# Kernel optimization log

Measured on AMD Instinct MI355X. Metric: run time of the kernel, lower is better.

## Reference

```python
import jax, jax.numpy as jnp
import numpy as np

N_NODES = 100000
D_FEAT = 128            # per-embedding width; concat of 4 -> 512
INPUT_DIM = 4 * D_FEAT
HIDDEN_DIM = 64
N_SAMPLES = 250000


def _glorot(key, fan_in, fan_out):
    r = np.sqrt(6.0 / fan_in).astype(np.float32)
    return jax.random.uniform(key, (fan_in, fan_out), minval=-r, maxval=r, dtype=jnp.float32)


def setup_inputs() -> dict:
    key = jax.random.key(0)
    k1, k2, k3, k4, k5 = jax.random.split(key, 5)
    input1 = jax.random.normal(k1, (N_NODES, D_FEAT), dtype=jnp.float32)
    input2 = jax.random.normal(k2, (N_NODES, D_FEAT), dtype=jnp.float32)
    train_sample = jax.random.randint(k3, (N_SAMPLES, 2), 0, N_NODES, dtype=jnp.int64)
    w1 = _glorot(k4, INPUT_DIM, HIDDEN_DIM)
    b1 = jnp.zeros((HIDDEN_DIM,), dtype=jnp.float32)
    w2 = _glorot(k5, HIDDEN_DIM, 1)
    return {"input1": input1, "input2": input2, "train_sample": train_sample,
            "w1": w1, "b1": b1, "w2": w2}


def reference(input1, input2, train_sample, w1, b1, w2):
    src = train_sample[:, 0]
    dst = train_sample[:, 1]
    # four gathers + concat -> [E, 4*D_FEAT]
    h = jnp.concatenate([input1[src], input1[dst], input2[src], input2[dst]], axis=1)
    x = jax.nn.relu(h @ w1 + b1)          # [E, HIDDEN_DIM]
    return x @ w2                          # [E, 1]
```

## Files before the change

kernel.cpp:

```cpp
#include <hip/hip_runtime.h>
#include <hip/hip_bf16.h>

#define NN  100000
#define DF  128
#define HD  64
#define NS  250000


typedef __attribute__((ext_vector_type(8))) short bfrag;
typedef __attribute__((ext_vector_type(4))) float ffrag;

__device__ __forceinline__ unsigned short bf16bits(float f) {
    __hip_bfloat16 b = __float2bfloat16(f);
    return *(unsigned short*)&b;
}
__device__ __forceinline__ unsigned pack2(float a, float b) {
    return (unsigned)bf16bits(a) | ((unsigned)bf16bits(b) << 16);
}
__device__ __forceinline__ float bflo(unsigned u) {
    union { unsigned i; float f; } c; c.i = u << 16; return c.f;
}
__device__ __forceinline__ float bfhi(unsigned u) {
    union { unsigned i; float f; } c; c.i = u & 0xffff0000u; return c.f;
}

__global__ __launch_bounds__(256) void prep_w1_kernel(
    const float* __restrict__ w1, const float* __restrict__ w2,
    unsigned short* __restrict__ Bf, unsigned short* __restrict__ w2bf)
{
    const int gid = blockIdx.x * 256 + threadIdx.x;
    if (gid >= 4096) {
        const int j = gid - 4096;
        if (j < HD) w2bf[j] = bf16bits(w2[j]);
        return;
    }
    const int lane = gid & 63;
    const int ks   = (gid >> 6) & 7;
    const int tn   = gid >> 9;

    const int n     = tn * 16 + (lane & 15);
    const int kbase = ks * 32 + (lane >> 4) * 8;
    const int col   = n & 63;

    uint4 u;
    unsigned p[4];
    #pragma unroll
    for (int jp = 0; jp < 4; ++jp) {
        float v[2];
        #pragma unroll
        for (int h = 0; h < 2; ++h) {
            const int k = kbase + jp * 2 + h;
            const int row = ((k >= 128) ? 256 : 0) + ((n >= 64) ? 128 : 0) + (k & 127);
            v[h] = w1[(size_t)row * HD + col];
        }
        p[jp] = pack2(v[0], v[1]);
    }
    u.x = p[0]; u.y = p[1]; u.z = p[2]; u.w = p[3];
    *(uint4*)(Bf + (size_t)gid * 8) = u;
}

__global__ __launch_bounds__(256) void node_gemm_mfma(
    const float* __restrict__ in1,
    const float* __restrict__ in2,
    const unsigned short* __restrict__ Bf,
    const float* __restrict__ b1,
    unsigned short* __restrict__ Pn)
{
    __shared__ unsigned short smem[20480];

    const int t  = threadIdx.x;
    const int m0 = blockIdx.x * 80;

    const int lane = t & 63;
    const int w    = t >> 6;
    bfrag bfr[2][8];
    #pragma unroll
    for (int ti = 0; ti < 2; ++ti) {
        const int tn = w * 2 + ti;
        #pragma unroll
        for (int ks = 0; ks < 8; ++ks)
            bfr[ti][ks] = *(const bfrag*)(Bf + ((size_t)(tn * 8 + ks) * 64 + lane) * 8);
    }

    {
        const int r  = t >> 4;
        const int qq = t & 15;
        #pragma unroll
        for (int st = 0; st < 5; ++st) {
            const int row = m0 + st * 16 + r;
            const float* src = (qq < 8)
                ? in1 + (size_t)row * DF + qq * 16
                : in2 + (size_t)row * DF + (qq - 8) * 16;
            const float4 f0 = *(const float4*)(src);
            const float4 f1 = *(const float4*)(src + 4);
            const float4 f2 = *(const float4*)(src + 8);
            const float4 f3 = *(const float4*)(src + 12);
            uint4 u0, u1;
            u0.x = pack2(f0.x, f0.y); u0.y = pack2(f0.z, f0.w);
            u0.z = pack2(f1.x, f1.y); u0.w = pack2(f1.z, f1.w);
            u1.x = pack2(f2.x, f2.y); u1.y = pack2(f2.z, f2.w);
            u1.z = pack2(f3.x, f3.y); u1.w = pack2(f3.z, f3.w);
            const int g0 = qq * 2, g1 = qq * 2 + 1;
            *(uint4*)(&smem[st * 4096 + (g0 >> 2) * 512 + ((g0 & 3) * 16 + r) * 8]) = u0;
            *(uint4*)(&smem[st * 4096 + (g1 >> 2) * 512 + ((g1 & 3) * 16 + r) * 8]) = u1;
        }
    }
    __syncthreads();

    ffrag acc[5][2];
    #pragma unroll
    for (int st = 0; st < 5; ++st) {
        acc[st][0] = (ffrag){0.f, 0.f, 0.f, 0.f};
        acc[st][1] = (ffrag){0.f, 0.f, 0.f, 0.f};
    }
    #pragma unroll
    for (int ks = 0; ks < 8; ++ks) {
        #pragma unroll
        for (int st = 0; st < 5; ++st) {
            const bfrag af = *(const bfrag*)(&smem[st * 4096 + ks * 512 + lane * 8]);
            acc[st][0] = __builtin_amdgcn_mfma_f32_16x16x32_bf16(af, bfr[0][ks], acc[st][0], 0, 0, 0);
            acc[st][1] = __builtin_amdgcn_mfma_f32_16x16x32_bf16(af, bfr[1][ks], acc[st][1], 0, 0, 0);
        }
    }

    __syncthreads();
    {
        const int col = lane & 15;
        const int rq  = lane >> 4;
        float badd[2];
        #pragma unroll
        for (int ti = 0; ti < 2; ++ti) {
            const int nc = (w * 2 + ti) * 16 + col;
            badd[ti] = (w < 2) ? b1[nc] : 0.f;
        }
        #pragma unroll
        for (int st = 0; st < 5; ++st) {
            #pragma unroll
            for (int ti = 0; ti < 2; ++ti) {
                const int nc = (w * 2 + ti) * 16 + col;
                #pragma unroll
                for (int reg = 0; reg < 4; ++reg)
                    smem[(st * 16 + rq * 4 + reg) * 128 + nc] =
                        bf16bits(acc[st][ti][reg] + badd[ti]);
            }
        }
    }
    __syncthreads();
    {
        #pragma unroll
        for (int i = 0; i < 5; ++i) {
            const int idx = i * 256 + t;
            const int row = idx >> 4;
            const int seg = idx & 15;
            const uint4 u = *(const uint4*)(&smem[row * 128 + seg * 8]);
            *(uint4*)(Pn + (size_t)(m0 + row) * 128 + seg * 8) = u;
        }
    }
}

__global__ __launch_bounds__(256) void edge_mlp_kernel(
    const unsigned short* __restrict__ Pn,
    const int*   __restrict__ ts,
    const unsigned short* __restrict__ w2bf,
    float* __restrict__ out)
{
    const int t  = threadIdx.x;
    const int sr = blockIdx.x * 32 + (t >> 3);
    const int s  = min(sr, NS - 1);
    const int l  = t & 7;
    const int j  = l * 8;

    const int2 e = ((const int2*)ts)[s];
    const uint4 uu = *(const uint4*)(Pn + (size_t)e.x * 128 + j);
    const uint4 vv = *(const uint4*)(Pn + (size_t)e.y * 128 + 64 + j);
    const uint4 ww = *(const uint4*)(w2bf + j);

    float p = 0.f, x;
    x = bflo(uu.x) + bflo(vv.x); x = x > 0.f ? x : 0.f; p += x * bflo(ww.x);
    x = bfhi(uu.x) + bfhi(vv.x); x = x > 0.f ? x : 0.f; p += x * bfhi(ww.x);
    x = bflo(uu.y) + bflo(vv.y); x = x > 0.f ? x : 0.f; p += x * bflo(ww.y);
    x = bfhi(uu.y) + bfhi(vv.y); x = x > 0.f ? x : 0.f; p += x * bfhi(ww.y);
    x = bflo(uu.z) + bflo(vv.z); x = x > 0.f ? x : 0.f; p += x * bflo(ww.z);
    x = bfhi(uu.z) + bfhi(vv.z); x = x > 0.f ? x : 0.f; p += x * bfhi(ww.z);
    x = bflo(uu.w) + bflo(vv.w); x = x > 0.f ? x : 0.f; p += x * bflo(ww.w);
    x = bfhi(uu.w) + bfhi(vv.w); x = x > 0.f ? x : 0.f; p += x * bfhi(ww.w);

    p += __shfl_xor(p, 1);
    p += __shfl_xor(p, 2);
    p += __shfl_xor(p, 4);
    if (l == 0 && sr < NS) out[sr] = p;
}

extern "C" void kernel_launch(void* const* d_in, const int* in_sizes, int n_in,
                              void* d_out, int out_size, void* d_ws, size_t ws_size,
                              hipStream_t stream) {
    const float* in1 = (const float*)d_in[0];
    const float* in2 = (const float*)d_in[1];
    const int*   ts  = (const int*)  d_in[2];
    const float* w1  = (const float*)d_in[3];
    const float* b1  = (const float*)d_in[4];
    const float* w2  = (const float*)d_in[5];
    float* out = (float*)d_out;

    unsigned short* Pn = (unsigned short*)d_ws;
    const size_t Pbytes = (size_t)NN * 128 * sizeof(unsigned short);
    unsigned short* Bf;
    unsigned short* w2bf;
    if (ws_size >= Pbytes + 65536 + 128) {
        Bf   = (unsigned short*)((char*)d_ws + Pbytes);
        w2bf = (unsigned short*)((char*)d_ws + Pbytes + 65536);
    } else {
        Bf   = (unsigned short*)d_out;
        w2bf = (unsigned short*)((char*)d_out + 65536);
    }

    prep_w1_kernel<<<17, 256, 0, stream>>>(w1, w2, Bf, w2bf);
    node_gemm_mfma<<<NN / 80, 256, 0, stream>>>(in1, in2, Bf, b1, Pn);
    edge_mlp_kernel<<<(NS + 31) / 32, 256, 0, stream>>>(Pn, ts, w2bf, out);
}
```

Baseline: 148.5 us.

## Feed node GEMM MFMA directly from global loads, dropping LDS staging

The node GEMM kernel no longer stages converted input rows and output tiles through shared memory. Each wave loads its node rows straight from global memory into MFMA B-fragments, and with swapped operands the accumulators come out transposed, so each lane writes four consecutive output columns as one 8-byte store. Block size drops from 80 to 32 nodes, giving more blocks and removing the barriers, at the cost of every wave redundantly reading the same input rows (four times per block) and less coalesced global stores.

```diff
diff --git a/kernel.cpp b/kernel.cpp
--- a/kernel.cpp
+++ b/kernel.cpp
@@ -66,94 +66,66 @@
     const float* __restrict__ b1,
     unsigned short* __restrict__ Pn)
 {
-    __shared__ unsigned short smem[20480];
-
-    const int t  = threadIdx.x;
-    const int m0 = blockIdx.x * 80;
-
+    const int t    = threadIdx.x;
     const int lane = t & 63;
     const int w    = t >> 6;
-    bfrag bfr[2][8];
+    const int m0   = blockIdx.x * 32;
+
+    bfrag wf[2][8];
     #pragma unroll
     for (int ti = 0; ti < 2; ++ti) {
         const int tn = w * 2 + ti;
         #pragma unroll
         for (int ks = 0; ks < 8; ++ks)
-            bfr[ti][ks] = *(const bfrag*)(Bf + ((size_t)(tn * 8 + ks) * 64 + lane) * 8);
+            wf[ti][ks] = *(const bfrag*)(Bf + ((size_t)(tn * 8 + ks) * 64 + lane) * 8);
     }
 
-    {
-        const int r  = t >> 4;
-        const int qq = t & 15;
+    const int rq = lane >> 4;
+    float4 badd[2];
+    #pragma unroll
+    for (int ti = 0; ti < 2; ++ti) {
+        const int c0 = w * 32 + ti * 16 + rq * 4;
+        badd[ti] = (w < 2) ? *(const float4*)(b1 + c0)
+                           : make_float4(0.f, 0.f, 0.f, 0.f);
+    }
+
+    ffrag acc[2][2];
+    #pragma unroll
+    for (int rg = 0; rg < 2; ++rg) {
+        acc[rg][0] = (ffrag){0.f, 0.f, 0.f, 0.f};
+        acc[rg][1] = (ffrag){0.f, 0.f, 0.f, 0.f};
+    }
+
+    #pragma unroll
+    for (int rg = 0; rg < 2; ++rg) {
+        const int row = m0 + rg * 16 + (lane & 15);
+        const float* r1 = in1 + (size_t)row * DF;
+        const float* r2 = in2 + (size_t)row * DF;
         #pragma unroll
-        for (int st = 0; st < 5; ++st) {
-            const int row = m0 + st * 16 + r;
-            const float* src = (qq < 8)
-                ? in1 + (size_t)row * DF + qq * 16
-                : in2 + (size_t)row * DF + (qq - 8) * 16;
+        for (int ks = 0; ks < 8; ++ks) {
+            const float* src = (ks < 4) ? r1 + ks * 32 + rq * 8
+                                        : r2 + (ks - 4) * 32 + rq * 8;
             const float4 f0 = *(const float4*)(src);
             const float4 f1 = *(const float4*)(src + 4);
-            const float4 f2 = *(const float4*)(src + 8);
-            const float4 f3 = *(const float4*)(src + 12);
-            uint4 u0, u1;
-            u0.x = pack2(f0.x, f0.y); u0.y = pack2(f0.z, f0.w);
-            u0.z = pack2(f1.x, f1.y); u0.w = pack2(f1.z, f1.w);
-            u1.x = pack2(f2.x, f2.y); u1.y = pack2(f2.z, f2.w);
-            u1.z = pack2(f3.x, f3.y); u1.w = pack2(f3.z, f3.w);
-            const int g0 = qq * 2, g1 = qq * 2 + 1;
-            *(uint4*)(&smem[st * 4096 + (g0 >> 2) * 512 + ((g0 & 3) * 16 + r) * 8]) = u0;
-            *(uint4*)(&smem[st * 4096 + (g1 >> 2) * 512 + ((g1 & 3) * 16 + r) * 8]) = u1;
-        }
-    }
-    __syncthreads();
-
-    ffrag acc[5][2];
-    #pragma unroll
-    for (int st = 0; st < 5; ++st) {
-        acc[st][0] = (ffrag){0.f, 0.f, 0.f, 0.f};
-        acc[st][1] = (ffrag){0.f, 0.f, 0.f, 0.f};
-    }
-    #pragma unroll
-    for (int ks = 0; ks < 8; ++ks) {
-        #pragma unroll
-        for (int st = 0; st < 5; ++st) {
-            const bfrag af = *(const bfrag*)(&smem[st * 4096 + ks * 512 + lane * 8]);
-            acc[st][0] = __builtin_amdgcn_mfma_f32_16x16x32_bf16(af, bfr[0][ks], acc[st][0], 0, 0, 0);
-            acc[st][1] = __builtin_amdgcn_mfma_f32_16x16x32_bf16(af, bfr[1][ks], acc[st][1], 0, 0, 0);
+            bfrag nf;
+            uint4* nu = (uint4*)&nf;
+            nu->x = pack2(f0.x, f0.y); nu->y = pack2(f0.z, f0.w);
+            nu->z = pack2(f1.x, f1.y); nu->w = pack2(f1.z, f1.w);
+            acc[rg][0] = __builtin_amdgcn_mfma_f32_16x16x32_bf16(wf[0][ks], nf, acc[rg][0], 0, 0, 0);
+            acc[rg][1] = __builtin_amdgcn_mfma_f32_16x16x32_bf16(wf[1][ks], nf, acc[rg][1], 0, 0, 0);
         }
     }
 
-    __syncthreads();
-    {
-        const int col = lane & 15;
-        const int rq  = lane >> 4;
-        float badd[2];
+    #pragma unroll
+    for (int rg = 0; rg < 2; ++rg) {
+        const int nrow = m0 + rg * 16 + (lane & 15);
         #pragma unroll
         for (int ti = 0; ti < 2; ++ti) {
-            const int nc = (w * 2 + ti) * 16 + col;
-            badd[ti] = (w < 2) ? b1[nc] : 0.f;
-        }
-        #pragma unroll
-        for (int st = 0; st < 5; ++st) {
-            #pragma unroll
-            for (int ti = 0; ti < 2; ++ti) {
-                const int nc = (w * 2 + ti) * 16 + col;
-                #pragma unroll
-                for (int reg = 0; reg < 4; ++reg)
-                    smem[(st * 16 + rq * 4 + reg) * 128 + nc] =
-                        bf16bits(acc[st][ti][reg] + badd[ti]);
-            }
-        }
-    }
-    __syncthreads();
-    {
-        #pragma unroll
-        for (int i = 0; i < 5; ++i) {
-            const int idx = i * 256 + t;
-            const int row = idx >> 4;
-            const int seg = idx & 15;
-            const uint4 u = *(const uint4*)(&smem[row * 128 + seg * 8]);
-            *(uint4*)(Pn + (size_t)(m0 + row) * 128 + seg * 8) = u;
+            const int c0 = w * 32 + ti * 16 + rq * 4;
+            uint2 u;
+            u.x = pack2(acc[rg][ti][0] + badd[ti].x, acc[rg][ti][1] + badd[ti].y);
+            u.y = pack2(acc[rg][ti][2] + badd[ti].z, acc[rg][ti][3] + badd[ti].w);
+            *(uint2*)(Pn + (size_t)nrow * 128 + c0) = u;
         }
     }
 }
@@ -215,6 +187,6 @@
     }
 
     prep_w1_kernel<<<17, 256, 0, stream>>>(w1, w2, Bf, w2bf);
-    node_gemm_mfma<<<NN / 80, 256, 0, stream>>>(in1, in2, Bf, b1, Pn);
+    node_gemm_mfma<<<NN / 32, 256, 0, stream>>>(in1, in2, Bf, b1, Pn);
     edge_mlp_kernel<<<(NS + 31) / 32, 256, 0, stream>>>(Pn, ts, w2bf, out);
 }
```

New measurement: 184.0 us. +23.9%, slower.

## Software-pipeline node GEMM tiles with register prefetch and double-buffered LDS

Applied to the files above, without the earlier changes.

The node GEMM kernel now processes its five 16-row tiles one at a time. It prefetches the next tile's fp32 rows into registers while the current tile is converted, stored to a double-buffered LDS area and run through MFMA. Each wave writes its own slice of the output through a small per-wave LDS staging buffer, which removes two block-wide barriers. A custom barrier waits only on LDS counters so that in-flight global prefetches are not drained. This relies on subtle barrier correctness across the reused double buffer, and it keeps more registers live.

```diff
diff --git a/kernel.cpp b/kernel.cpp
--- a/kernel.cpp
+++ b/kernel.cpp
@@ -22,6 +22,10 @@
 }
 __device__ __forceinline__ float bfhi(unsigned u) {
     union { unsigned i; float f; } c; c.i = u & 0xffff0000u; return c.f;
+}
+__device__ __forceinline__ void barrier_lgkm_only() {
+    __builtin_amdgcn_s_waitcnt(0xC07F);
+    __builtin_amdgcn_s_barrier();
 }
 
 __global__ __launch_bounds__(256) void prep_w1_kernel(
@@ -59,6 +63,9 @@
     *(uint4*)(Bf + (size_t)gid * 8) = u;
 }
 
+#define NTILE 5
+#define NBLK  (NN / (16 * NTILE))
+
 __global__ __launch_bounds__(256) void node_gemm_mfma(
     const float* __restrict__ in1,
     const float* __restrict__ in2,
@@ -66,13 +73,15 @@
     const float* __restrict__ b1,
     unsigned short* __restrict__ Pn)
 {
-    __shared__ unsigned short smem[20480];
-
-    const int t  = threadIdx.x;
-    const int m0 = blockIdx.x * 80;
-
+    __shared__ unsigned short smem[8192 + 4 * 576];
+
+    const int t    = threadIdx.x;
     const int lane = t & 63;
     const int w    = t >> 6;
+
+    const int r  = t >> 4;
+    const int qq = t & 15;
+
     bfrag bfr[2][8];
     #pragma unroll
     for (int ti = 0; ti < 2; ++ti) {
@@ -81,80 +90,84 @@
         for (int ks = 0; ks < 8; ++ks)
             bfr[ti][ks] = *(const bfrag*)(Bf + ((size_t)(tn * 8 + ks) * 64 + lane) * 8);
     }
-
+    float badd[2];
+    #pragma unroll
+    for (int ti = 0; ti < 2; ++ti) {
+        const int nc = w * 32 + ti * 16 + (lane & 15);
+        badd[ti] = (w < 2) ? b1[nc] : 0.f;
+    }
+
+    const int tile0 = blockIdx.x * NTILE;
+
+    float4 f0, f1, f2, f3;
     {
-        const int r  = t >> 4;
-        const int qq = t & 15;
-        #pragma unroll
-        for (int st = 0; st < 5; ++st) {
-            const int row = m0 + st * 16 + r;
+        const int row = (tile0)*16 + r;
+        const float* src = (qq < 8)
+            ? in1 + (size_t)row * DF + qq * 16
+            : in2 + (size_t)row * DF + (qq - 8) * 16;
+        f0 = *(const float4*)(src);
+        f1 = *(const float4*)(src + 4);
+        f2 = *(const float4*)(src + 8);
+        f3 = *(const float4*)(src + 12);
+    }
+
+    #pragma unroll
+    for (int it = 0; it < NTILE; ++it) {
+        const int m0 = (tile0 + it) * 16;
+
+        float4 g0, g1, g2, g3;
+        {
+            const int nt  = (it + 1 < NTILE) ? (tile0 + it + 1) : tile0;
+            const int row = nt * 16 + r;
             const float* src = (qq < 8)
                 ? in1 + (size_t)row * DF + qq * 16
                 : in2 + (size_t)row * DF + (qq - 8) * 16;
-            const float4 f0 = *(const float4*)(src);
-            const float4 f1 = *(const float4*)(src + 4);
-            const float4 f2 = *(const float4*)(src + 8);
-            const float4 f3 = *(const float4*)(src + 12);
+            g0 = *(const float4*)(src);
+            g1 = *(const float4*)(src + 4);
+            g2 = *(const float4*)(src + 8);
+            g3 = *(const float4*)(src + 12);
+        }
+
+        unsigned short* abuf = &smem[(it & 1) * 4096];
+        {
             uint4 u0, u1;
             u0.x = pack2(f0.x, f0.y); u0.y = pack2(f0.z, f0.w);
             u0.z = pack2(f1.x, f1.y); u0.w = pack2(f1.z, f1.w);
             u1.x = pack2(f2.x, f2.y); u1.y = pack2(f2.z, f2.w);
             u1.z = pack2(f3.x, f3.y); u1.w = pack2(f3.z, f3.w);
-            const int g0 = qq * 2, g1 = qq * 2 + 1;
-            *(uint4*)(&smem[st * 4096 + (g0 >> 2) * 512 + ((g0 & 3) * 16 + r) * 8]) = u0;
-            *(uint4*)(&smem[st * 4096 + (g1 >> 2) * 512 + ((g1 & 3) * 16 + r) * 8]) = u1;
-        }
-    }
-    __syncthreads();
-
-    ffrag acc[5][2];
-    #pragma unroll
-    for (int st = 0; st < 5; ++st) {
-        acc[st][0] = (ffrag){0.f, 0.f, 0.f, 0.f};
-        acc[st][1] = (ffrag){0.f, 0.f, 0.f, 0.f};
-    }
-    #pragma unroll
-    for (int ks = 0; ks < 8; ++ks) {
+            const int g0i = qq * 2, g1i = qq * 2 + 1;
+            *(uint4*)(&abuf[(g0i >> 2) * 512 + ((g0i & 3) * 16 + r) * 8]) = u0;
+            *(uint4*)(&abuf[(g1i >> 2) * 512 + ((g1i & 3) * 16 + r) * 8]) = u1;
+        }
+
+        barrier_lgkm_only();
+
+        ffrag acc[2] = {{0.f, 0.f, 0.f, 0.f}, {0.f, 0.f, 0.f, 0.f}};
         #pragma unroll
-        for (int st = 0; st < 5; ++st) {
-            const bfrag af = *(const bfrag*)(&smem[st * 4096 + ks * 512 + lane * 8]);
-            acc[st][0] = __builtin_amdgcn_mfma_f32_16x16x32_bf16(af, bfr[0][ks], acc[st][0], 0, 0, 0);
-            acc[st][1] = __builtin_amdgcn_mfma_f32_16x16x32_bf16(af, bfr[1][ks], acc[st][1], 0, 0, 0);
-        }
-    }
-
-    __syncthreads();
-    {
-        const int col = lane & 15;
-        const int rq  = lane >> 4;
-        float badd[2];
-        #pragma unroll
-        for (int ti = 0; ti < 2; ++ti) {
-            const int nc = (w * 2 + ti) * 16 + col;
-            badd[ti] = (w < 2) ? b1[nc] : 0.f;
-        }
-        #pragma unroll
-        for (int st = 0; st < 5; ++st) {
+        for (int ks = 0; ks < 8; ++ks) {
+            const bfrag af = *(const bfrag*)(&abuf[ks * 512 + lane * 8]);
+            acc[0] = __builtin_amdgcn_mfma_f32_16x16x32_bf16(af, bfr[0][ks], acc[0], 0, 0, 0);
+            acc[1] = __builtin_amdgcn_mfma_f32_16x16x32_bf16(af, bfr[1][ks], acc[1], 0, 0, 0);
+        }
+
+        {
+            unsigned short* ep = &smem[8192 + w * 576];
+            const int col = lane & 15;
+            const int rq  = lane >> 4;
             #pragma unroll
             for (int ti = 0; ti < 2; ++ti) {
-                const int nc = (w * 2 + ti) * 16 + col;
                 #pragma unroll
                 for (int reg = 0; reg < 4; ++reg)
-                    smem[(st * 16 + rq * 4 + reg) * 128 + nc] =
-                        bf16bits(acc[st][ti][reg] + badd[ti]);
+                    ep[(rq * 4 + reg) * 36 + ti * 16 + col] =
+                        bf16bits(acc[ti][reg] + badd[ti]);
             }
-        }
-    }
-    __syncthreads();
-    {
-        #pragma unroll
-        for (int i = 0; i < 5; ++i) {
-            const int idx = i * 256 + t;
-            const int row = idx >> 4;
-            const int seg = idx & 15;
-            const uint4 u = *(const uint4*)(&smem[row * 128 + seg * 8]);
-            *(uint4*)(Pn + (size_t)(m0 + row) * 128 + seg * 8) = u;
-        }
+            const int rowm = lane >> 2;
+            const int seg  = lane & 3;
+            const uint4 u = *(const uint4*)(&ep[rowm * 36 + seg * 8]);
+            *(uint4*)(Pn + (size_t)(m0 + rowm) * 128 + w * 32 + seg * 8) = u;
+        }
+
+        f0 = g0; f1 = g1; f2 = g2; f3 = g3;
     }
 }
 
@@ -215,6 +228,6 @@
     }
 
     prep_w1_kernel<<<17, 256, 0, stream>>>(w1, w2, Bf, w2bf);
-    node_gemm_mfma<<<NN / 80, 256, 0, stream>>>(in1, in2, Bf, b1, Pn);
+    node_gemm_mfma<<<NBLK, 256, 0, stream>>>(in1, in2, Bf, b1, Pn);
     edge_mlp_kernel<<<(NS + 31) / 32, 256, 0, stream>>>(Pn, ts, w2bf, out);
 }
```

Measured after the change: 148.9 us. About the same (+0.3%).
